# Performance work log

Measured on AMD Instinct MI355X. Metric: run time of the kernel, lower is better.

Reference implementation:

```python
import jax, jax.numpy as jnp
import numpy as np

B, S, E, A, DK, H = 8, 2048, 256, 16, 64, 64  # batch, seq, embed, action, d_key, mlp hidden


def setup_inputs() -> dict:
    key = jax.random.key(0)
    ks = jax.random.split(key, 8)
    obs = jax.random.normal(ks[0], (B, S, E), dtype=jnp.float32)
    act = jnp.zeros((B, S, A), dtype=jnp.float32)  # one-hot actions; unused by forward
    # projection weights stored as [in, out] (torch Linear applies x @ W.T)
    Wq = jax.random.normal(ks[1], (E, DK), dtype=jnp.float32) / np.sqrt(E)
    Wk = jax.random.normal(ks[2], (E, DK), dtype=jnp.float32) / np.sqrt(E)
    Wv = jax.random.normal(ks[3], (E, DK), dtype=jnp.float32) / np.sqrt(E)
    W1 = jax.random.normal(ks[4], (DK, H), dtype=jnp.float32) / np.sqrt(DK)
    b1 = jnp.zeros((H,), dtype=jnp.float32)
    W2 = jax.random.normal(ks[5], (H, 1), dtype=jnp.float32) / np.sqrt(H)
    b2 = jnp.zeros((1,), dtype=jnp.float32)
    return dict(obs=obs, act=act, Wq=Wq, Wk=Wk, Wv=Wv, W1=W1, b1=b1, W2=W2, b2=b2)


def reference(obs, act, Wq, Wk, Wv, W1, b1, W2, b2):
    b, s, _ = obs.shape
    dk = Wq.shape[1]
    scale = dk ** -0.25  # applied to both q and k, net 1/sqrt(dk)
    q = (obs @ Wq) * scale          # [b, s, dk]
    k = (obs @ Wk) * scale          # [b, s, dk]
    v = obs @ Wv                    # [b, s, dk]
    scores = jnp.einsum('bqd,bkd->bqk', q, k)  # [b, s, s]
    causal = jnp.tril(jnp.ones((s, s), dtype=bool))
    scores = jnp.where(causal[None], scores, -jnp.inf)
    attn = jax.nn.softmax(scores, axis=2)      # [b, s, s]
    attn_out = jnp.einsum('bqk,bkd->bqd', attn, v)  # [b, s, dk]
    h = jax.nn.relu(attn_out.reshape(b * s, dk) @ W1 + b1)
    x = h @ W2 + b2                 # [b*s, 1]
    return (x, attn)
```

## Files before the change

kernel.cpp:

```cpp
#include <hip/hip_runtime.h>
#include <hip/hip_bf16.h>
#include <math.h>

#define NB 8
#define SQ 2048
#define EMB 256
#define DK 64
#define HID 64

typedef __attribute__((ext_vector_type(8))) short short8;
typedef __attribute__((ext_vector_type(4))) float f32x4;

__device__ __forceinline__ short f2bf(float f) {
    union { float f; unsigned u; } v; v.f = f;
    unsigned r = v.u + 0x7FFF + ((v.u >> 16) & 1);
    return (short)(r >> 16);
}

__global__ __launch_bounds__(256) void k_cvt_obs(const float* __restrict__ obs,
                                                 short* __restrict__ out, int n) {
    int i = (blockIdx.x * 256 + threadIdx.x) * 4;
    if (i >= n) return;
    float4 v = *(const float4*)(obs + i);
    short4 o;
    o.x = f2bf(v.x); o.y = f2bf(v.y); o.z = f2bf(v.z); o.w = f2bf(v.w);
    *(short4*)(out + i) = o;
}

__global__ __launch_bounds__(256) void k_wt(const float* __restrict__ Wq,
                                            const float* __restrict__ Wk,
                                            const float* __restrict__ Wv,
                                            short* __restrict__ wt) {
    int o = blockIdx.x * 256 + threadIdx.x;
    int row = o >> 8, e = o & 255;
    int w = row >> 6, d = row & 63;
    const float* W = (w == 0) ? Wq : ((w == 1) ? Wk : Wv);
    wt[o] = f2bf(W[e * 64 + d]);
}

__global__ __launch_bounds__(256) void k_proj(const short* __restrict__ obsb,
                                              const short* __restrict__ wt,
                                              short* __restrict__ qw,
                                              short* __restrict__ kw,
                                              short* __restrict__ vt) {
    int tid = threadIdx.x, w = tid >> 6, l = tid & 63;
    int rb = blockIdx.x;
    int r0 = rb * 64 + w * 16;
    int arow = r0 + (l & 15);
    int eo = (l >> 4) * 8;
    f32x4 acc[12];
    #pragma unroll
    for (int c = 0; c < 12; ++c) acc[c] = (f32x4){0.f, 0.f, 0.f, 0.f};
    #pragma unroll
    for (int ks = 0; ks < 8; ++ks) {
        int e0 = ks * 32;
        short8 a = *(const short8*)(obsb + (size_t)arow * 256 + e0 + eo);
        #pragma unroll
        for (int c = 0; c < 12; ++c) {
            short8 bf = *(const short8*)(wt + (size_t)(c * 16 + (l & 15)) * 256 + e0 + eo);
            acc[c] = __builtin_amdgcn_mfma_f32_16x16x32_bf16(a, bf, acc[c], 0, 0, 0);
        }
    }
    const float scale = 0.35355339059327373f;
    __shared__ short ldsv[64][72];
    int rloc = w * 16 + (l >> 4) * 4;
    int col16 = l & 15;
    #pragma unroll
    for (int c = 0; c < 12; ++c) {
        #pragma unroll
        for (int r = 0; r < 4; ++r) {
            float val = acc[c][r];
            int row = r0 + (l >> 4) * 4 + r;
            if (c < 4) {
                qw[(size_t)row * 64 + c * 16 + col16] = f2bf(val * scale);
            } else if (c < 8) {
                kw[(size_t)row * 64 + (c - 4) * 16 + col16] = f2bf(val * scale);
            } else {
                ldsv[(c - 8) * 16 + col16][rloc + r] = f2bf(val);
            }
        }
    }
    __syncthreads();
    int b = (rb * 64) >> 11;
    int s0 = (rb * 64) & 2047;
    int d = tid >> 2, ch = (tid & 3) * 16;
    short* dst = vt + (size_t)b * 64 * 2048 + (size_t)d * 2048 + s0 + ch;
    #pragma unroll
    for (int j = 0; j < 16; ++j) dst[j] = ldsv[d][ch + j];
}

__global__ __launch_bounds__(256) void k_qkt(const short* __restrict__ qw,
                                             const short* __restrict__ kw,
                                             float* __restrict__ attn) {
    int t = blockIdx.x;
    int b = blockIdx.y;
    int qb = (int)((sqrtf(8.f * t + 1.f) - 1.f) * 0.5f);
    while ((qb + 1) * (qb + 2) / 2 <= t) qb++;
    while (qb * (qb + 1) / 2 > t) qb--;
    int kb = t - qb * (qb + 1) / 2;
    int q0 = qb * 64, k0 = kb * 64;
    int tid = threadIdx.x, w = tid >> 6, l = tid & 63;
    int wr = w >> 1, wc = w & 1;
    int eo = (l >> 4) * 8;
    const short* qbase = qw + (size_t)b * SQ * 64;
    const short* kbase = kw + (size_t)b * SQ * 64;
    f32x4 acc[2][2];
    #pragma unroll
    for (int mi = 0; mi < 2; ++mi)
        #pragma unroll
        for (int nj = 0; nj < 2; ++nj) acc[mi][nj] = (f32x4){0.f, 0.f, 0.f, 0.f};
    #pragma unroll
    for (int ks = 0; ks < 2; ++ks) {
        short8 a[2], bb[2];
        #pragma unroll
        for (int mi = 0; mi < 2; ++mi)
            a[mi] = *(const short8*)(qbase + (size_t)(q0 + wr * 32 + mi * 16 + (l & 15)) * 64 + ks * 32 + eo);
        #pragma unroll
        for (int nj = 0; nj < 2; ++nj)
            bb[nj] = *(const short8*)(kbase + (size_t)(k0 + wc * 32 + nj * 16 + (l & 15)) * 64 + ks * 32 + eo);
        #pragma unroll
        for (int mi = 0; mi < 2; ++mi)
            #pragma unroll
            for (int nj = 0; nj < 2; ++nj)
                acc[mi][nj] = __builtin_amdgcn_mfma_f32_16x16x32_bf16(a[mi], bb[nj], acc[mi][nj], 0, 0, 0);
    }
    float* abase = attn + (size_t)b * SQ * SQ;
    #pragma unroll
    for (int mi = 0; mi < 2; ++mi)
        #pragma unroll
        for (int nj = 0; nj < 2; ++nj)
            #pragma unroll
            for (int r = 0; r < 4; ++r) {
                int row = q0 + wr * 32 + mi * 16 + (l >> 4) * 4 + r;
                int col = k0 + wc * 32 + nj * 16 + (l & 15);
                abase[(size_t)row * SQ + col] = acc[mi][nj][r];
            }
}

__global__ __launch_bounds__(256) void k_softmax(float* __restrict__ attn) {
    int q = blockIdx.x, b = blockIdx.y;
    int tid = threadIdx.x, w = tid >> 6, l = tid & 63;
    float* row = attn + ((size_t)b * SQ + q) * SQ;
    int c0 = tid * 8;
    float4 v0 = *(const float4*)(row + c0);
    float4 v1 = *(const float4*)(row + c0 + 4);
    float s[8] = {v0.x, v0.y, v0.z, v0.w, v1.x, v1.y, v1.z, v1.w};
    float lm = -INFINITY;
    #pragma unroll
    for (int j = 0; j < 8; ++j) {
        if (c0 + j > q) s[j] = -INFINITY;
        lm = fmaxf(lm, s[j]);
    }
    #pragma unroll
    for (int o = 32; o > 0; o >>= 1) lm = fmaxf(lm, __shfl_xor(lm, o));
    __shared__ float red[8];
    if (l == 0) red[w] = lm;
    __syncthreads();
    float m = fmaxf(fmaxf(red[0], red[1]), fmaxf(red[2], red[3]));
    float ls = 0.f;
    #pragma unroll
    for (int j = 0; j < 8; ++j) { s[j] = __expf(s[j] - m); ls += s[j]; }
    #pragma unroll
    for (int o = 32; o > 0; o >>= 1) ls += __shfl_xor(ls, o);
    if (l == 0) red[4 + w] = ls;
    __syncthreads();
    float tot = red[4] + red[5] + red[6] + red[7];
    float inv = 1.f / tot;
    float4 o0, o1;
    o0.x = s[0] * inv; o0.y = s[1] * inv; o0.z = s[2] * inv; o0.w = s[3] * inv;
    o1.x = s[4] * inv; o1.y = s[5] * inv; o1.z = s[6] * inv; o1.w = s[7] * inv;
    *(float4*)(row + c0) = o0;
    *(float4*)(row + c0 + 4) = o1;
}

__global__ __launch_bounds__(256) void k_pv(const float* __restrict__ attn,
                                            const short* __restrict__ vt,
                                            float* __restrict__ ao) {
    int rb = blockIdx.x, b = blockIdx.y;
    int q0 = rb * 64;
    int tid = threadIdx.x, w = tid >> 6, l = tid & 63;
    int r0 = q0 + w * 16;
    const float* abase = attn + (size_t)b * SQ * SQ;
    const short* vbase = vt + (size_t)b * 64 * SQ;
    int eo = (l >> 4) * 8;
    f32x4 acc[4];
    #pragma unroll
    for (int nj = 0; nj < 4; ++nj) acc[nj] = (f32x4){0.f, 0.f, 0.f, 0.f};
    int arow = r0 + (l & 15);
    int kmax = q0 + 64;
    for (int k0 = 0; k0 < kmax; k0 += 32) {
        const float* ap = abase + (size_t)arow * SQ + k0 + eo;
        float4 a0 = *(const float4*)ap;
        float4 a1 = *(const float4*)(ap + 4);
        short8 af;
        af[0] = f2bf(a0.x); af[1] = f2bf(a0.y); af[2] = f2bf(a0.z); af[3] = f2bf(a0.w);
        af[4] = f2bf(a1.x); af[5] = f2bf(a1.y); af[6] = f2bf(a1.z); af[7] = f2bf(a1.w);
        #pragma unroll
        for (int nj = 0; nj < 4; ++nj) {
            short8 bf = *(const short8*)(vbase + (size_t)(nj * 16 + (l & 15)) * SQ + k0 + eo);
            acc[nj] = __builtin_amdgcn_mfma_f32_16x16x32_bf16(af, bf, acc[nj], 0, 0, 0);
        }
    }
    #pragma unroll
    for (int nj = 0; nj < 4; ++nj)
        #pragma unroll
        for (int r = 0; r < 4; ++r) {
            size_t grow = (size_t)b * SQ + r0 + (l >> 4) * 4 + r;
            ao[grow * 64 + nj * 16 + (l & 15)] = acc[nj][r];
        }
}

__global__ __launch_bounds__(256) void k_mlp(const float* __restrict__ ao,
                                             const float* __restrict__ W1,
                                             const float* __restrict__ b1,
                                             const float* __restrict__ W2,
                                             const float* __restrict__ b2,
                                             float* __restrict__ x) {
    int tid = threadIdx.x, w = tid >> 6, l = tid & 63;
    int grow = blockIdx.x * 4 + w;
    __shared__ float lds[4][64];
    lds[w][l] = ao[(size_t)grow * 64 + l];
    __syncthreads();
    float acc = b1[l];
    #pragma unroll
    for (int d = 0; d < 64; ++d) acc += lds[w][d] * W1[d * 64 + l];
    float h = fmaxf(acc, 0.f);
    float p = h * W2[l];
    #pragma unroll
    for (int o = 32; o > 0; o >>= 1) p += __shfl_xor(p, o);
    if (l == 0) x[grow] = p + b2[0];
}

extern "C" void kernel_launch(void* const* d_in, const int* in_sizes, int n_in,
                              void* d_out, int out_size, void* d_ws, size_t ws_size,
                              hipStream_t stream) {
    const float* obs = (const float*)d_in[0];
    const float* Wq  = (const float*)d_in[2];
    const float* Wk  = (const float*)d_in[3];
    const float* Wv  = (const float*)d_in[4];
    const float* W1  = (const float*)d_in[5];
    const float* b1  = (const float*)d_in[6];
    const float* W2  = (const float*)d_in[7];
    const float* b2  = (const float*)d_in[8];

    float* x    = (float*)d_out;
    float* attn = (float*)d_out + NB * SQ;

    char* ws = (char*)d_ws;
    short* obsb = (short*)(ws);
    short* wt   = (short*)(ws + 8388608);
    short* qw   = (short*)(ws + 8486912);
    short* kw   = (short*)(ws + 10584064);
    short* vt   = (short*)(ws + 12681216);
    float* ao   = (float*)(ws + 14778368);

    k_cvt_obs<<<dim3(4096), dim3(256), 0, stream>>>(obs, obsb, NB * SQ * EMB);
    k_wt<<<dim3(192), dim3(256), 0, stream>>>(Wq, Wk, Wv, wt);
    k_proj<<<dim3(256), dim3(256), 0, stream>>>(obsb, wt, qw, kw, vt);
    k_qkt<<<dim3(528, NB), dim3(256), 0, stream>>>(qw, kw, attn);
    k_softmax<<<dim3(SQ, NB), dim3(256), 0, stream>>>(attn);
    k_pv<<<dim3(32, NB), dim3(256), 0, stream>>>(attn, vt, ao);
    k_mlp<<<dim3(4096), dim3(256), 0, stream>>>(ao, W1, b1, W2, b2, x);
}
```

Before: 141.9 us.

## Replace QK^T/softmax/PV passes with flash attention plus single attn-write pass

Replaces the separate score, softmax and PV kernels with a flash-style kernel that computes the attention output using an online softmax and saves per-row max and inverse sum. A second kernel recomputes QK^T per tile and writes the normalized attention probabilities (zeros above the diagonal) exactly once. The attention matrix is no longer written, read back, rewritten and read again. The bf16 conversion of obs is also folded into the projection kernel, dropping one launch and an intermediate buffer. In exchange QK^T is computed twice, and the flash kernel has only 256 blocks with causal load imbalance.

```diff
diff --git a/kernel.cpp b/kernel.cpp
--- a/kernel.cpp
+++ b/kernel.cpp
@@ -5,8 +5,6 @@
 #define NB 8
 #define SQ 2048
 #define EMB 256
-#define DK 64
-#define HID 64
 
 typedef __attribute__((ext_vector_type(8))) short short8;
 typedef __attribute__((ext_vector_type(4))) float f32x4;
@@ -15,16 +13,6 @@
     union { float f; unsigned u; } v; v.f = f;
     unsigned r = v.u + 0x7FFF + ((v.u >> 16) & 1);
     return (short)(r >> 16);
-}
-
-__global__ __launch_bounds__(256) void k_cvt_obs(const float* __restrict__ obs,
-                                                 short* __restrict__ out, int n) {
-    int i = (blockIdx.x * 256 + threadIdx.x) * 4;
-    if (i >= n) return;
-    float4 v = *(const float4*)(obs + i);
-    short4 o;
-    o.x = f2bf(v.x); o.y = f2bf(v.y); o.z = f2bf(v.z); o.w = f2bf(v.w);
-    *(short4*)(out + i) = o;
 }
 
 __global__ __launch_bounds__(256) void k_wt(const float* __restrict__ Wq,
@@ -38,7 +26,7 @@
     wt[o] = f2bf(W[e * 64 + d]);
 }
 
-__global__ __launch_bounds__(256) void k_proj(const short* __restrict__ obsb,
+__global__ __launch_bounds__(256) void k_proj(const float* __restrict__ obs,
                                               const short* __restrict__ wt,
                                               short* __restrict__ qw,
                                               short* __restrict__ kw,
@@ -54,7 +42,12 @@
     #pragma unroll
     for (int ks = 0; ks < 8; ++ks) {
         int e0 = ks * 32;
-        short8 a = *(const short8*)(obsb + (size_t)arow * 256 + e0 + eo);
+        const float* ap = obs + (size_t)arow * 256 + e0 + eo;
+        float4 f0 = *(const float4*)ap;
+        float4 f1 = *(const float4*)(ap + 4);
+        short8 a;
+        a[0] = f2bf(f0.x); a[1] = f2bf(f0.y); a[2] = f2bf(f0.z); a[3] = f2bf(f0.w);
+        a[4] = f2bf(f1.x); a[5] = f2bf(f1.y); a[6] = f2bf(f1.z); a[7] = f2bf(f1.w);
         #pragma unroll
         for (int c = 0; c < 12; ++c) {
             short8 bf = *(const short8*)(wt + (size_t)(c * 16 + (l & 15)) * 256 + e0 + eo);
@@ -89,125 +82,148 @@
     for (int j = 0; j < 16; ++j) dst[j] = ldsv[d][ch + j];
 }
 
-__global__ __launch_bounds__(256) void k_qkt(const short* __restrict__ qw,
-                                             const short* __restrict__ kw,
-                                             float* __restrict__ attn) {
-    int t = blockIdx.x;
-    int b = blockIdx.y;
-    int qb = (int)((sqrtf(8.f * t + 1.f) - 1.f) * 0.5f);
-    while ((qb + 1) * (qb + 2) / 2 <= t) qb++;
-    while (qb * (qb + 1) / 2 > t) qb--;
-    int kb = t - qb * (qb + 1) / 2;
-    int q0 = qb * 64, k0 = kb * 64;
+__global__ __launch_bounds__(256) void k_flash(const short* __restrict__ qw,
+                                               const short* __restrict__ kw,
+                                               const short* __restrict__ vt,
+                                               float* __restrict__ ao,
+                                               float* __restrict__ ml) {
+    int qb = blockIdx.x, b = blockIdx.y;
+    int q0 = qb * 64;
     int tid = threadIdx.x, w = tid >> 6, l = tid & 63;
-    int wr = w >> 1, wc = w & 1;
-    int eo = (l >> 4) * 8;
+    int lg = l >> 4, lc = l & 15;
+    int r0 = q0 + w * 16;
+    int eo = lg * 8;
+    __shared__ short ldsP[4][16][72];
     const short* qbase = qw + (size_t)b * SQ * 64;
     const short* kbase = kw + (size_t)b * SQ * 64;
-    f32x4 acc[2][2];
-    #pragma unroll
-    for (int mi = 0; mi < 2; ++mi)
-        #pragma unroll
-        for (int nj = 0; nj < 2; ++nj) acc[mi][nj] = (f32x4){0.f, 0.f, 0.f, 0.f};
-    #pragma unroll
-    for (int ks = 0; ks < 2; ++ks) {
-        short8 a[2], bb[2];
-        #pragma unroll
-        for (int mi = 0; mi < 2; ++mi)
-            a[mi] = *(const short8*)(qbase + (size_t)(q0 + wr * 32 + mi * 16 + (l & 15)) * 64 + ks * 32 + eo);
-        #pragma unroll
-        for (int nj = 0; nj < 2; ++nj)
-            bb[nj] = *(const short8*)(kbase + (size_t)(k0 + wc * 32 + nj * 16 + (l & 15)) * 64 + ks * 32 + eo);
-        #pragma unroll
-        for (int mi = 0; mi < 2; ++mi)
-            #pragma unroll
-            for (int nj = 0; nj < 2; ++nj)
-                acc[mi][nj] = __builtin_amdgcn_mfma_f32_16x16x32_bf16(a[mi], bb[nj], acc[mi][nj], 0, 0, 0);
-    }
+    const short* vbase = vt + (size_t)b * 64 * SQ;
+    short8 qf0 = *(const short8*)(qbase + (size_t)(r0 + lc) * 64 + eo);
+    short8 qf1 = *(const short8*)(qbase + (size_t)(r0 + lc) * 64 + 32 + eo);
+    float m[4], lsum[4];
+    f32x4 o[4];
+    #pragma unroll
+    for (int r = 0; r < 4; ++r) { m[r] = -INFINITY; lsum[r] = 0.f; }
+    #pragma unroll
+    for (int nj = 0; nj < 4; ++nj) o[nj] = (f32x4){0.f, 0.f, 0.f, 0.f};
+
+    for (int kb = 0; kb <= qb; ++kb) {
+        int k0 = kb * 64;
+        f32x4 s[4];
+        #pragma unroll
+        for (int nj = 0; nj < 4; ++nj) s[nj] = (f32x4){0.f, 0.f, 0.f, 0.f};
+        #pragma unroll
+        for (int nj = 0; nj < 4; ++nj) {
+            short8 kf = *(const short8*)(kbase + (size_t)(k0 + nj * 16 + lc) * 64 + eo);
+            s[nj] = __builtin_amdgcn_mfma_f32_16x16x32_bf16(qf0, kf, s[nj], 0, 0, 0);
+        }
+        #pragma unroll
+        for (int nj = 0; nj < 4; ++nj) {
+            short8 kf = *(const short8*)(kbase + (size_t)(k0 + nj * 16 + lc) * 64 + 32 + eo);
+            s[nj] = __builtin_amdgcn_mfma_f32_16x16x32_bf16(qf1, kf, s[nj], 0, 0, 0);
+        }
+        if (kb == qb) {
+            #pragma unroll
+            for (int nj = 0; nj < 4; ++nj)
+                #pragma unroll
+                for (int r = 0; r < 4; ++r)
+                    if (k0 + nj * 16 + lc > r0 + lg * 4 + r) s[nj][r] = -INFINITY;
+        }
+        #pragma unroll
+        for (int r = 0; r < 4; ++r) {
+            float pm = fmaxf(fmaxf(s[0][r], s[1][r]), fmaxf(s[2][r], s[3][r]));
+            pm = fmaxf(pm, __shfl_xor(pm, 1));
+            pm = fmaxf(pm, __shfl_xor(pm, 2));
+            pm = fmaxf(pm, __shfl_xor(pm, 4));
+            pm = fmaxf(pm, __shfl_xor(pm, 8));
+            float mn = fmaxf(m[r], pm);
+            float sc = __expf(m[r] - mn);
+            m[r] = mn;
+            lsum[r] *= sc;
+            #pragma unroll
+            for (int nj = 0; nj < 4; ++nj) o[nj][r] *= sc;
+            float ps = 0.f;
+            #pragma unroll
+            for (int nj = 0; nj < 4; ++nj) {
+                float p = __expf(s[nj][r] - mn);
+                ps += p;
+                ldsP[w][lg * 4 + r][nj * 16 + lc] = f2bf(p);
+            }
+            ps += __shfl_xor(ps, 1);
+            ps += __shfl_xor(ps, 2);
+            ps += __shfl_xor(ps, 4);
+            ps += __shfl_xor(ps, 8);
+            lsum[r] += ps;
+        }
+        #pragma unroll
+        for (int ks = 0; ks < 2; ++ks) {
+            short8 pa = *(const short8*)&ldsP[w][lc][ks * 32 + lg * 8];
+            #pragma unroll
+            for (int nj = 0; nj < 4; ++nj) {
+                short8 vf = *(const short8*)(vbase + (size_t)(nj * 16 + lc) * SQ + k0 + ks * 32 + eo);
+                o[nj] = __builtin_amdgcn_mfma_f32_16x16x32_bf16(pa, vf, o[nj], 0, 0, 0);
+            }
+        }
+    }
+    #pragma unroll
+    for (int r = 0; r < 4; ++r) {
+        float inv = 1.f / lsum[r];
+        int row = r0 + lg * 4 + r;
+        if (lc == 0) {
+            ml[((size_t)b * SQ + row) * 2]     = m[r];
+            ml[((size_t)b * SQ + row) * 2 + 1] = inv;
+        }
+        #pragma unroll
+        for (int nj = 0; nj < 4; ++nj)
+            ao[((size_t)b * SQ + row) * 64 + nj * 16 + lc] = o[nj][r] * inv;
+    }
+}
+
+__global__ __launch_bounds__(256) void k_attnw(const short* __restrict__ qw,
+                                               const short* __restrict__ kw,
+                                               const float* __restrict__ ml,
+                                               float* __restrict__ attn) {
+    int kb = blockIdx.x, qb = blockIdx.y, b = blockIdx.z;
+    int q0 = qb * 64, k0 = kb * 64;
     float* abase = attn + (size_t)b * SQ * SQ;
-    #pragma unroll
-    for (int mi = 0; mi < 2; ++mi)
-        #pragma unroll
-        for (int nj = 0; nj < 2; ++nj)
-            #pragma unroll
-            for (int r = 0; r < 4; ++r) {
-                int row = q0 + wr * 32 + mi * 16 + (l >> 4) * 4 + r;
-                int col = k0 + wc * 32 + nj * 16 + (l & 15);
-                abase[(size_t)row * SQ + col] = acc[mi][nj][r];
-            }
-}
-
-__global__ __launch_bounds__(256) void k_softmax(float* __restrict__ attn) {
-    int q = blockIdx.x, b = blockIdx.y;
-    int tid = threadIdx.x, w = tid >> 6, l = tid & 63;
-    float* row = attn + ((size_t)b * SQ + q) * SQ;
-    int c0 = tid * 8;
-    float4 v0 = *(const float4*)(row + c0);
-    float4 v1 = *(const float4*)(row + c0 + 4);
-    float s[8] = {v0.x, v0.y, v0.z, v0.w, v1.x, v1.y, v1.z, v1.w};
-    float lm = -INFINITY;
-    #pragma unroll
-    for (int j = 0; j < 8; ++j) {
-        if (c0 + j > q) s[j] = -INFINITY;
-        lm = fmaxf(lm, s[j]);
-    }
-    #pragma unroll
-    for (int o = 32; o > 0; o >>= 1) lm = fmaxf(lm, __shfl_xor(lm, o));
-    __shared__ float red[8];
-    if (l == 0) red[w] = lm;
-    __syncthreads();
-    float m = fmaxf(fmaxf(red[0], red[1]), fmaxf(red[2], red[3]));
-    float ls = 0.f;
-    #pragma unroll
-    for (int j = 0; j < 8; ++j) { s[j] = __expf(s[j] - m); ls += s[j]; }
-    #pragma unroll
-    for (int o = 32; o > 0; o >>= 1) ls += __shfl_xor(ls, o);
-    if (l == 0) red[4 + w] = ls;
-    __syncthreads();
-    float tot = red[4] + red[5] + red[6] + red[7];
-    float inv = 1.f / tot;
-    float4 o0, o1;
-    o0.x = s[0] * inv; o0.y = s[1] * inv; o0.z = s[2] * inv; o0.w = s[3] * inv;
-    o1.x = s[4] * inv; o1.y = s[5] * inv; o1.z = s[6] * inv; o1.w = s[7] * inv;
-    *(float4*)(row + c0) = o0;
-    *(float4*)(row + c0 + 4) = o1;
-}
-
-__global__ __launch_bounds__(256) void k_pv(const float* __restrict__ attn,
-                                            const short* __restrict__ vt,
-                                            float* __restrict__ ao) {
-    int rb = blockIdx.x, b = blockIdx.y;
-    int q0 = rb * 64;
-    int tid = threadIdx.x, w = tid >> 6, l = tid & 63;
-    int r0 = q0 + w * 16;
-    const float* abase = attn + (size_t)b * SQ * SQ;
-    const short* vbase = vt + (size_t)b * 64 * SQ;
-    int eo = (l >> 4) * 8;
-    f32x4 acc[4];
-    #pragma unroll
-    for (int nj = 0; nj < 4; ++nj) acc[nj] = (f32x4){0.f, 0.f, 0.f, 0.f};
-    int arow = r0 + (l & 15);
-    int kmax = q0 + 64;
-    for (int k0 = 0; k0 < kmax; k0 += 32) {
-        const float* ap = abase + (size_t)arow * SQ + k0 + eo;
-        float4 a0 = *(const float4*)ap;
-        float4 a1 = *(const float4*)(ap + 4);
-        short8 af;
-        af[0] = f2bf(a0.x); af[1] = f2bf(a0.y); af[2] = f2bf(a0.z); af[3] = f2bf(a0.w);
-        af[4] = f2bf(a1.x); af[5] = f2bf(a1.y); af[6] = f2bf(a1.z); af[7] = f2bf(a1.w);
+    int tid = threadIdx.x;
+    if (kb > qb) {
+        int row = q0 + (tid >> 2);
+        float4* dst = (float4*)(abase + (size_t)row * SQ + k0 + (tid & 3) * 16);
+        float4 z = {0.f, 0.f, 0.f, 0.f};
+        dst[0] = z; dst[1] = z; dst[2] = z; dst[3] = z;
+        return;
+    }
+    int w = tid >> 6, l = tid & 63, lg = l >> 4, lc = l & 15;
+    int r0 = q0 + w * 16, eo = lg * 8;
+    const short* qbase = qw + (size_t)b * SQ * 64;
+    const short* kbase = kw + (size_t)b * SQ * 64;
+    short8 qf0 = *(const short8*)(qbase + (size_t)(r0 + lc) * 64 + eo);
+    short8 qf1 = *(const short8*)(qbase + (size_t)(r0 + lc) * 64 + 32 + eo);
+    f32x4 s[4];
+    #pragma unroll
+    for (int nj = 0; nj < 4; ++nj) s[nj] = (f32x4){0.f, 0.f, 0.f, 0.f};
+    #pragma unroll
+    for (int nj = 0; nj < 4; ++nj) {
+        short8 kf = *(const short8*)(kbase + (size_t)(k0 + nj * 16 + lc) * 64 + eo);
+        s[nj] = __builtin_amdgcn_mfma_f32_16x16x32_bf16(qf0, kf, s[nj], 0, 0, 0);
+    }
+    #pragma unroll
+    for (int nj = 0; nj < 4; ++nj) {
+        short8 kf = *(const short8*)(kbase + (size_t)(k0 + nj * 16 + lc) * 64 + 32 + eo);
+        s[nj] = __builtin_amdgcn_mfma_f32_16x16x32_bf16(qf1, kf, s[nj], 0, 0, 0);
+    }
+    #pragma unroll
+    for (int r = 0; r < 4; ++r) {
+        int row = r0 + lg * 4 + r;
+        float mr = ml[((size_t)b * SQ + row) * 2];
+        float iv = ml[((size_t)b * SQ + row) * 2 + 1];
         #pragma unroll
         for (int nj = 0; nj < 4; ++nj) {
-            short8 bf = *(const short8*)(vbase + (size_t)(nj * 16 + (l & 15)) * SQ + k0 + eo);
-            acc[nj] = __builtin_amdgcn_mfma_f32_16x16x32_bf16(af, bf, acc[nj], 0, 0, 0);
-        }
-    }
-    #pragma unroll
-    for (int nj = 0; nj < 4; ++nj)
-        #pragma unroll
-        for (int r = 0; r < 4; ++r) {
-            size_t grow = (size_t)b * SQ + r0 + (l >> 4) * 4 + r;
-            ao[grow * 64 + nj * 16 + (l & 15)] = acc[nj][r];
-        }
+            int col = k0 + nj * 16 + lc;
+            float p = (col <= row) ? __expf(s[nj][r] - mr) * iv : 0.f;
+            abase[(size_t)row * SQ + col] = p;
+        }
+    }
 }
 
 __global__ __launch_bounds__(256) void k_mlp(const float* __restrict__ ao,
@@ -247,18 +263,16 @@
     float* attn = (float*)d_out + NB * SQ;
 
     char* ws = (char*)d_ws;
-    short* obsb = (short*)(ws);
-    short* wt   = (short*)(ws + 8388608);
-    short* qw   = (short*)(ws + 8486912);
-    short* kw   = (short*)(ws + 10584064);
-    short* vt   = (short*)(ws + 12681216);
-    float* ao   = (float*)(ws + 14778368);
-
-    k_cvt_obs<<<dim3(4096), dim3(256), 0, stream>>>(obs, obsb, NB * SQ * EMB);
+    short* wt = (short*)(ws);
+    short* qw = (short*)(ws + 131072);
+    short* kw = (short*)(ws + 2228224);
+    short* vt = (short*)(ws + 4325376);
+    float* ml = (float*)(ws + 6422528);
+    float* ao = (float*)(ws + 6553600);
+
     k_wt<<<dim3(192), dim3(256), 0, stream>>>(Wq, Wk, Wv, wt);
-    k_proj<<<dim3(256), dim3(256), 0, stream>>>(obsb, wt, qw, kw, vt);
-    k_qkt<<<dim3(528, NB), dim3(256), 0, stream>>>(qw, kw, attn);
-    k_softmax<<<dim3(SQ, NB), dim3(256), 0, stream>>>(attn);
-    k_pv<<<dim3(32, NB), dim3(256), 0, stream>>>(attn, vt, ao);
+    k_proj<<<dim3(256), dim3(256), 0, stream>>>(obs, wt, qw, kw, vt);
+    k_flash<<<dim3(32, NB), dim3(256), 0, stream>>>(qw, kw, vt, ao, ml);
+    k_attnw<<<dim3(32, 32, NB), dim3(256), 0, stream>>>(qw, kw, ml, attn);
     k_mlp<<<dim3(4096), dim3(256), 0, stream>>>(ao, W1, b1, W2, b2, x);
 }
```

New measurement: 152.4 us. 7.4% more time.
